# Kernel optimization log

Hardware: AMD Instinct MI355X
Metric: run time of the kernel (lower is better)

## Reference

```python
import jax, jax.numpy as jnp
import numpy as np

NEG_INF = -1.0e9  # matches torch masked_fill value (unused: no mask)

def setup_inputs() -> dict:
    key = jax.random.key(0)
    kq, kk, kv = jax.random.split(key, 3)
    B, Sq, Sk, D = 8, 2048, 2048, 512
    return {
        "query": jax.random.normal(kq, (B, Sq, D), dtype=jnp.float32),
        "key": jax.random.normal(kk, (B, Sk, D), dtype=jnp.float32),
        "value": jax.random.normal(kv, (B, Sk, D), dtype=jnp.float32),
        "temperature": jnp.ones((), dtype=jnp.float32),
    }

def reference(query, key, value, temperature):
    # Squared Euclidean distance via GEMM identity: ||q||^2 + ||k||^2 - 2 q.k
    # (same math as the broadcast sum((q-k)^2, -1), but without [B,Sq,Sk,D] tensor)
    q_sq = jnp.sum(query * query, axis=-1, keepdims=True)          # [B,Sq,1]
    k_sq = jnp.sum(key * key, axis=-1)[:, None, :]                 # [B,1,Sk]
    qk = jnp.einsum("bqd,bkd->bqk", query, key)                    # [B,Sq,Sk]
    distance_squared = q_sq + k_sq - 2.0 * qk
    similarity = -distance_squared / temperature
    attention_weights = jax.nn.softmax(similarity, axis=-1)        # [B,Sq,Sk]
    attended_values = jnp.einsum("bqk,bkd->bqd", attention_weights, value)
    return attended_values, attention_weights
```

## Files before the change

kernel.cpp:

```cpp
#include <hip/hip_runtime.h>

typedef __bf16 bf16_t;
typedef __bf16 bf16x8 __attribute__((ext_vector_type(8)));
typedef __bf16 bf16x4 __attribute__((ext_vector_type(4)));
typedef __bf16 bf16x2 __attribute__((ext_vector_type(2)));
typedef float f32x4 __attribute__((ext_vector_type(4)));

#define NB 8
#define SQ 2048
#define SK 2048
#define DD 512

#define BM 128
#define BN 128
#define BK 32
#define LDK 40
#define NBLK (SK / BN)

__global__ __launch_bounds__(256, 2) void logits_kernel(
    const float* __restrict__ Q, const float* __restrict__ K,
    const float* __restrict__ tempP, float* __restrict__ logits,
    float* __restrict__ Mpart, float* __restrict__ Spart) {
  __shared__ bf16_t qh[BM][LDK], ql[BM][LDK], kh[BN][LDK], kl[BN][LDK];
  __shared__ float ksred[BN][8];
  __shared__ float mred[BM][2], sred[BM][2];
  const int b = blockIdx.z;
  const int m0 = blockIdx.y * BM;
  const int n0 = blockIdx.x * BN;
  const int tid = threadIdx.x;
  const int lane = tid & 63;
  const int wave = tid >> 6;
  const int wm = (wave >> 1) * 64;
  const int wn = (wave & 1) * 64;
  const int lrow = lane & 15;
  const int quad = lane >> 4;

  const float* Qb = Q + (size_t)b * SQ * DD;
  const float* Kb = K + (size_t)b * SK * DD;

  const int srow = tid >> 3;
  const int scol = (tid & 7) * 4;

  const float* qbase = Qb + (size_t)(m0 + srow) * DD + scol;
  const float* kbase = Kb + (size_t)(n0 + srow) * DD + scol;

  f32x4 acc[4][4];
#pragma unroll
  for (int i = 0; i < 4; i++)
#pragma unroll
    for (int j = 0; j < 4; j++) acc[i][j] = (f32x4){0.f, 0.f, 0.f, 0.f};

  float kss[4] = {0.f, 0.f, 0.f, 0.f};

  float4 pq[4], pk[4];
#pragma unroll
  for (int i = 0; i < 4; i++) {
    pq[i] = *(const float4*)(qbase + (size_t)i * 32 * DD);
    pk[i] = *(const float4*)(kbase + (size_t)i * 32 * DD);
  }

  for (int k0 = 0; k0 < DD; k0 += BK) {
    __syncthreads();
#pragma unroll
    for (int i = 0; i < 4; i++) {
      const int r = srow + i * 32;
      float4 qv = pq[i], kv = pk[i];
      bf16_t q0 = (bf16_t)qv.x, q1 = (bf16_t)qv.y, q2 = (bf16_t)qv.z, q3 = (bf16_t)qv.w;
      bf16x4 qhv = {q0, q1, q2, q3};
      bf16x4 qlv = {(bf16_t)(qv.x - (float)q0), (bf16_t)(qv.y - (float)q1),
                    (bf16_t)(qv.z - (float)q2), (bf16_t)(qv.w - (float)q3)};
      bf16_t c0 = (bf16_t)kv.x, c1 = (bf16_t)kv.y, c2 = (bf16_t)kv.z, c3 = (bf16_t)kv.w;
      bf16x4 khv = {c0, c1, c2, c3};
      bf16x4 klv = {(bf16_t)(kv.x - (float)c0), (bf16_t)(kv.y - (float)c1),
                    (bf16_t)(kv.z - (float)c2), (bf16_t)(kv.w - (float)c3)};
      *(bf16x4*)&qh[r][scol] = qhv;
      *(bf16x4*)&ql[r][scol] = qlv;
      *(bf16x4*)&kh[r][scol] = khv;
      *(bf16x4*)&kl[r][scol] = klv;
      kss[i] = fmaf(kv.x, kv.x, kss[i]);
      kss[i] = fmaf(kv.y, kv.y, kss[i]);
      kss[i] = fmaf(kv.z, kv.z, kss[i]);
      kss[i] = fmaf(kv.w, kv.w, kss[i]);
    }
    __syncthreads();

    if (k0 + BK < DD) {
#pragma unroll
      for (int i = 0; i < 4; i++) {
        pq[i] = *(const float4*)(qbase + (size_t)i * 32 * DD + (k0 + BK));
        pk[i] = *(const float4*)(kbase + (size_t)i * 32 * DD + (k0 + BK));
      }
    }

    bf16x8 bh[4], bl[4];
#pragma unroll
    for (int ni = 0; ni < 4; ni++) {
      bh[ni] = *(const bf16x8*)&kh[wn + ni * 16 + lrow][quad * 8];
      bl[ni] = *(const bf16x8*)&kl[wn + ni * 16 + lrow][quad * 8];
    }
#pragma unroll
    for (int mi = 0; mi < 4; mi++) {
      bf16x8 ah = *(const bf16x8*)&qh[wm + mi * 16 + lrow][quad * 8];
      bf16x8 al = *(const bf16x8*)&ql[wm + mi * 16 + lrow][quad * 8];
#pragma unroll
      for (int ni = 0; ni < 4; ni++) {
        acc[mi][ni] = __builtin_amdgcn_mfma_f32_16x16x32_bf16(ah, bh[ni], acc[mi][ni], 0, 0, 0);
        acc[mi][ni] = __builtin_amdgcn_mfma_f32_16x16x32_bf16(ah, bl[ni], acc[mi][ni], 0, 0, 0);
        acc[mi][ni] = __builtin_amdgcn_mfma_f32_16x16x32_bf16(al, bh[ni], acc[mi][ni], 0, 0, 0);
      }
    }
  }

#pragma unroll
  for (int i = 0; i < 4; i++) ksred[srow + i * 32][tid & 7] = kss[i];
  __syncthreads();

  const float invT = 1.0f / tempP[0];
  float* Lb = logits + (size_t)b * SQ * SK;
  float ks4[4];
#pragma unroll
  for (int ni = 0; ni < 4; ni++) {
    const float* kr = ksred[wn + ni * 16 + lrow];
    ks4[ni] = ((kr[0] + kr[1]) + (kr[2] + kr[3])) +
              ((kr[4] + kr[5]) + (kr[6] + kr[7]));
  }

#pragma unroll
  for (int mi = 0; mi < 4; mi++) {
#pragma unroll
    for (int r = 0; r < 4; r++) {
      const int row = wm + mi * 16 + quad * 4 + r;
      float sv[4];
#pragma unroll
      for (int ni = 0; ni < 4; ni++) {
        sv[ni] = (2.0f * acc[mi][ni][r] - ks4[ni]) * invT;
        Lb[(size_t)(m0 + row) * SK + (n0 + wn + ni * 16 + lrow)] = sv[ni];
      }
      float rm = fmaxf(fmaxf(sv[0], sv[1]), fmaxf(sv[2], sv[3]));
      rm = fmaxf(rm, __shfl_xor(rm, 1));
      rm = fmaxf(rm, __shfl_xor(rm, 2));
      rm = fmaxf(rm, __shfl_xor(rm, 4));
      rm = fmaxf(rm, __shfl_xor(rm, 8));
      float rs = __expf(sv[0] - rm) + __expf(sv[1] - rm) +
                 __expf(sv[2] - rm) + __expf(sv[3] - rm);
      rs += __shfl_xor(rs, 1);
      rs += __shfl_xor(rs, 2);
      rs += __shfl_xor(rs, 4);
      rs += __shfl_xor(rs, 8);
      if (lrow == 0) {
        mred[row][wave & 1] = rm;
        sred[row][wave & 1] = rs;
      }
    }
  }
  __syncthreads();
  if (tid < BM) {
    const float ma = mred[tid][0], mb = mred[tid][1];
    const float M = fmaxf(ma, mb);
    const float S = sred[tid][0] * __expf(ma - M) + sred[tid][1] * __expf(mb - M);
    const size_t o = ((size_t)b * NBLK + blockIdx.x) * SQ + (m0 + tid);
    Mpart[o] = M;
    Spart[o] = S;
  }
}

__global__ __launch_bounds__(256) void vt_kernel(const float* __restrict__ V,
                                                 bf16_t* __restrict__ Vt) {
  const int b = blockIdx.y;
  const int k0 = blockIdx.x * 32;
  const int tid = threadIdx.x;
  const int p = tid & 15;
  const int c = tid >> 4;
  const float* Vb = V + (size_t)b * SK * DD;
  bf16_t* Vtb = Vt + (size_t)b * DD * SK;
  const int k = k0 + 2 * p;
#pragma unroll
  for (int j = 0; j < 8; j++) {
    const int d0 = 4 * c + 64 * j;
    float4 v0 = *(const float4*)(Vb + (size_t)k * DD + d0);
    float4 v1 = *(const float4*)(Vb + (size_t)(k + 1) * DD + d0);
    bf16x2 t0 = {(bf16_t)v0.x, (bf16_t)v1.x};
    bf16x2 t1 = {(bf16_t)v0.y, (bf16_t)v1.y};
    bf16x2 t2 = {(bf16_t)v0.z, (bf16_t)v1.z};
    bf16x2 t3 = {(bf16_t)v0.w, (bf16_t)v1.w};
    *(bf16x2*)(Vtb + (size_t)(d0 + 0) * SK + k) = t0;
    *(bf16x2*)(Vtb + (size_t)(d0 + 1) * SK + k) = t1;
    *(bf16x2*)(Vtb + (size_t)(d0 + 2) * SK + k) = t2;
    *(bf16x2*)(Vtb + (size_t)(d0 + 3) * SK + k) = t3;
  }
}

#define PM 32

__device__ __forceinline__ unsigned lds_addr(int row, unsigned kb) {
  return (unsigned)row * 4096u + (kb ^ (unsigned)((row & 7) << 4));
}

__global__ __launch_bounds__(512, 1) void pv_kernel(
    float* __restrict__ L,
    const bf16_t* __restrict__ Vt,
    const float* __restrict__ Mpart, const float* __restrict__ Spart,
    float* __restrict__ O) {
  __shared__ __align__(16) unsigned char wlds[PM * 4096];
  __shared__ float Msh[PM], Ssh[PM];
  const int bid = blockIdx.x;
  const int b = bid & 7;
  const int m0 = (bid >> 3) * PM;
  const int tid = threadIdx.x;

  float* Lb = L + (size_t)b * SQ * SK;
  const bf16_t* Vtb = Vt + (size_t)b * DD * SK;

  {
    const int row = tid >> 4;
    const int j = tid & 15;
    const size_t o = ((size_t)b * NBLK + j) * SQ + (m0 + row);
    const float pm = Mpart[o];
    const float ps = Spart[o];
    float m = pm;
    m = fmaxf(m, __shfl_xor(m, 1));
    m = fmaxf(m, __shfl_xor(m, 2));
    m = fmaxf(m, __shfl_xor(m, 4));
    m = fmaxf(m, __shfl_xor(m, 8));
    float s = ps * __expf(pm - m);
    s += __shfl_xor(s, 1);
    s += __shfl_xor(s, 2);
    s += __shfl_xor(s, 4);
    s += __shfl_xor(s, 8);
    if (j == 0) {
      Msh[row] = m;
      Ssh[row] = 1.0f / s;
    }
  }
  __syncthreads();

  {
    const int row = tid >> 4;
    const int g = tid & 15;
    float* lp = Lb + (size_t)(m0 + row) * SK;
    const float M = Msh[row];
    const float invS = Ssh[row];
#pragma unroll 8
    for (int j = 0; j < 32; j++) {
      const int k = g * 4 + j * 64;
      float4 v = *(const float4*)(lp + k);
      const float w0 = __expf(v.x - M) * invS;
      const float w1 = __expf(v.y - M) * invS;
      const float w2 = __expf(v.z - M) * invS;
      const float w3 = __expf(v.w - M) * invS;
      *(float4*)(lp + k) = make_float4(w0, w1, w2, w3);
      bf16x4 w4 = {(bf16_t)w0, (bf16_t)w1, (bf16_t)w2, (bf16_t)w3};
      *(bf16x4*)(wlds + lds_addr(row, (unsigned)(k * 2))) = w4;
    }
  }
  __syncthreads();

  const int lane = tid & 63;
  const int wave = tid >> 6;
  const int wn = wave * 64;
  const int lrow = lane & 15;
  const int quad = lane >> 4;

  const bf16_t* Brow[4];
#pragma unroll
  for (int ni = 0; ni < 4; ni++)
    Brow[ni] = Vtb + (size_t)(wn + ni * 16 + lrow) * SK + quad * 8;

  f32x4 acc[2][4];
#pragma unroll
  for (int i = 0; i < 2; i++)
#pragma unroll
    for (int j = 0; j < 4; j++) acc[i][j] = (f32x4){0.f, 0.f, 0.f, 0.f};

  bf16x8 b0[4], b1[4];
#pragma unroll
  for (int ni = 0; ni < 4; ni++) b0[ni] = *(const bf16x8*)(Brow[ni]);
#pragma unroll
  for (int ni = 0; ni < 4; ni++) b1[ni] = *(const bf16x8*)(Brow[ni] + BK);

  for (int k0 = 0; k0 < SK; k0 += 2 * BK) {
    bf16x8 a0[2], a1[2];
#pragma unroll
    for (int mi = 0; mi < 2; mi++) {
      const int row = mi * 16 + lrow;
      a0[mi] = *(const bf16x8*)(wlds + lds_addr(row, (unsigned)((k0 + quad * 8) * 2)));
      a1[mi] = *(const bf16x8*)(wlds + lds_addr(row, (unsigned)((k0 + BK + quad * 8) * 2)));
    }
#pragma unroll
    for (int mi = 0; mi < 2; mi++)
#pragma unroll
      for (int ni = 0; ni < 4; ni++)
        acc[mi][ni] = __builtin_amdgcn_mfma_f32_16x16x32_bf16(a0[mi], b0[ni],
                                                              acc[mi][ni], 0, 0, 0);
    if (k0 + 2 * BK < SK) {
#pragma unroll
      for (int ni = 0; ni < 4; ni++)
        b0[ni] = *(const bf16x8*)(Brow[ni] + k0 + 2 * BK);
    }
#pragma unroll
    for (int mi = 0; mi < 2; mi++)
#pragma unroll
      for (int ni = 0; ni < 4; ni++)
        acc[mi][ni] = __builtin_amdgcn_mfma_f32_16x16x32_bf16(a1[mi], b1[ni],
                                                              acc[mi][ni], 0, 0, 0);
    if (k0 + 3 * BK < SK) {
#pragma unroll
      for (int ni = 0; ni < 4; ni++)
        b1[ni] = *(const bf16x8*)(Brow[ni] + k0 + 3 * BK);
    }
  }

  float* Ob = O + (size_t)b * SQ * DD;
#pragma unroll
  for (int ni = 0; ni < 4; ni++) {
    const int d = wn + ni * 16 + lrow;
#pragma unroll
    for (int mi = 0; mi < 2; mi++) {
      const int mbase = m0 + mi * 16 + quad * 4;
#pragma unroll
      for (int r = 0; r < 4; r++) {
        Ob[(size_t)(mbase + r) * DD + d] = acc[mi][ni][r];
      }
    }
  }
}

extern "C" void kernel_launch(void* const* d_in, const int* in_sizes, int n_in,
                              void* d_out, int out_size, void* d_ws, size_t ws_size,
                              hipStream_t stream) {
  const float* Q = (const float*)d_in[0];
  const float* K = (const float*)d_in[1];
  const float* V = (const float*)d_in[2];
  const float* T = (const float*)d_in[3];

  float* outv = (float*)d_out;
  float* logits = outv + (size_t)NB * SQ * DD;

  float* Mpart = (float*)d_ws;
  float* Spart = Mpart + (size_t)NB * NBLK * SQ;
  bf16_t* Vt = (bf16_t*)(Spart + (size_t)NB * NBLK * SQ);

  vt_kernel<<<dim3(SK / 32, NB), 256, 0, stream>>>(V, Vt);
  logits_kernel<<<dim3(SK / BN, SQ / BM, NB), 256, 0, stream>>>(Q, K, T, logits,
                                                                Mpart, Spart);
  pv_kernel<<<dim3(NB * (SQ / PM)), 512, 0, stream>>>(logits, Vt, Mpart, Spart, outv);
}
```

Baseline: 474.5 us.

## Pipeline softmax normalization with PV MFMA using chunked double-buffered LDS

The PV kernel no longer normalizes a whole 2048-wide row into a 128KB LDS buffer before any MFMA work. It now processes 256-wide chunks with a double-buffered 32KB LDS tile, prefetching the next chunk's logits while computing MFMAs on the current one, so global reads overlap with compute. The smaller LDS footprint allows more blocks per CU (launch bounds raised to 4). Logits are also pre-scaled by log2(e) so exp2f can replace __expf, at the cost of a log2-scaled intermediate and a hand-written barrier.

```diff
diff --git a/kernel.cpp b/kernel.cpp
--- a/kernel.cpp
+++ b/kernel.cpp
@@ -115,7 +115,7 @@
   for (int i = 0; i < 4; i++) ksred[srow + i * 32][tid & 7] = kss[i];
   __syncthreads();
 
-  const float invT = 1.0f / tempP[0];
+  const float invT = 1.4426950408889634f / tempP[0];
   float* Lb = logits + (size_t)b * SQ * SK;
   float ks4[4];
 #pragma unroll
@@ -141,8 +141,8 @@
       rm = fmaxf(rm, __shfl_xor(rm, 2));
       rm = fmaxf(rm, __shfl_xor(rm, 4));
       rm = fmaxf(rm, __shfl_xor(rm, 8));
-      float rs = __expf(sv[0] - rm) + __expf(sv[1] - rm) +
-                 __expf(sv[2] - rm) + __expf(sv[3] - rm);
+      float rs = exp2f(sv[0] - rm) + exp2f(sv[1] - rm) +
+                 exp2f(sv[2] - rm) + exp2f(sv[3] - rm);
       rs += __shfl_xor(rs, 1);
       rs += __shfl_xor(rs, 2);
       rs += __shfl_xor(rs, 4);
@@ -157,7 +157,7 @@
   if (tid < BM) {
     const float ma = mred[tid][0], mb = mred[tid][1];
     const float M = fmaxf(ma, mb);
-    const float S = sred[tid][0] * __expf(ma - M) + sred[tid][1] * __expf(mb - M);
+    const float S = sred[tid][0] * exp2f(ma - M) + sred[tid][1] * exp2f(mb - M);
     const size_t o = ((size_t)b * NBLK + blockIdx.x) * SQ + (m0 + tid);
     Mpart[o] = M;
     Spart[o] = S;
@@ -191,17 +191,21 @@
 }
 
 #define PM 32
-
-__device__ __forceinline__ unsigned lds_addr(int row, unsigned kb) {
-  return (unsigned)row * 4096u + (kb ^ (unsigned)((row & 7) << 4));
-}
-
-__global__ __launch_bounds__(512, 1) void pv_kernel(
+#define CK 256
+#define CKB 512
+#define NCH (SK / CK)
+#define NWIN (SK / BK)
+
+__device__ __forceinline__ unsigned pv_lds(int row, unsigned kb) {
+  return (unsigned)row * CKB + (kb ^ (unsigned)((row & 7) << 4));
+}
+
+__global__ __launch_bounds__(512, 4) void pv_kernel(
     float* __restrict__ L,
     const bf16_t* __restrict__ Vt,
     const float* __restrict__ Mpart, const float* __restrict__ Spart,
     float* __restrict__ O) {
-  __shared__ __align__(16) unsigned char wlds[PM * 4096];
+  __shared__ __align__(16) unsigned char wlds[2][PM * CKB];
   __shared__ float Msh[PM], Ssh[PM];
   const int bid = blockIdx.x;
   const int b = bid & 7;
@@ -222,7 +226,7 @@
     m = fmaxf(m, __shfl_xor(m, 2));
     m = fmaxf(m, __shfl_xor(m, 4));
     m = fmaxf(m, __shfl_xor(m, 8));
-    float s = ps * __expf(pm - m);
+    float s = ps * exp2f(pm - m);
     s += __shfl_xor(s, 1);
     s += __shfl_xor(s, 2);
     s += __shfl_xor(s, 4);
@@ -234,26 +238,28 @@
   }
   __syncthreads();
 
-  {
-    const int row = tid >> 4;
-    const int g = tid & 15;
-    float* lp = Lb + (size_t)(m0 + row) * SK;
-    const float M = Msh[row];
-    const float invS = Ssh[row];
-#pragma unroll 8
-    for (int j = 0; j < 32; j++) {
+  const int prow = tid >> 4;
+  const int g = tid & 15;
+  float* lp = Lb + (size_t)(m0 + prow) * SK;
+  const float Mrow = Msh[prow];
+  const float invS = Ssh[prow];
+
+  auto stage = [&](const float4 (&pv4)[4], int c1) {
+    unsigned char* buf = wlds[c1 & 1];
+    const int kbase = c1 * CK;
+#pragma unroll
+    for (int j = 0; j < 4; j++) {
       const int k = g * 4 + j * 64;
-      float4 v = *(const float4*)(lp + k);
-      const float w0 = __expf(v.x - M) * invS;
-      const float w1 = __expf(v.y - M) * invS;
-      const float w2 = __expf(v.z - M) * invS;
-      const float w3 = __expf(v.w - M) * invS;
-      *(float4*)(lp + k) = make_float4(w0, w1, w2, w3);
+      float4 v = pv4[j];
+      const float w0 = exp2f(v.x - Mrow) * invS;
+      const float w1 = exp2f(v.y - Mrow) * invS;
+      const float w2 = exp2f(v.z - Mrow) * invS;
+      const float w3 = exp2f(v.w - Mrow) * invS;
+      *(float4*)(lp + kbase + k) = make_float4(w0, w1, w2, w3);
       bf16x4 w4 = {(bf16_t)w0, (bf16_t)w1, (bf16_t)w2, (bf16_t)w3};
-      *(bf16x4*)(wlds + lds_addr(row, (unsigned)(k * 2))) = w4;
-    }
-  }
-  __syncthreads();
+      *(bf16x4*)(buf + pv_lds(prow, (unsigned)(k * 2))) = w4;
+    }
+  };
 
   const int lane = tid & 63;
   const int wave = tid >> 6;
@@ -272,41 +278,52 @@
 #pragma unroll
     for (int j = 0; j < 4; j++) acc[i][j] = (f32x4){0.f, 0.f, 0.f, 0.f};
 
-  bf16x8 b0[4], b1[4];
-#pragma unroll
-  for (int ni = 0; ni < 4; ni++) b0[ni] = *(const bf16x8*)(Brow[ni]);
-#pragma unroll
-  for (int ni = 0; ni < 4; ni++) b1[ni] = *(const bf16x8*)(Brow[ni] + BK);
-
-  for (int k0 = 0; k0 < SK; k0 += 2 * BK) {
-    bf16x8 a0[2], a1[2];
-#pragma unroll
-    for (int mi = 0; mi < 2; mi++) {
-      const int row = mi * 16 + lrow;
-      a0[mi] = *(const bf16x8*)(wlds + lds_addr(row, (unsigned)((k0 + quad * 8) * 2)));
-      a1[mi] = *(const bf16x8*)(wlds + lds_addr(row, (unsigned)((k0 + BK + quad * 8) * 2)));
-    }
-#pragma unroll
-    for (int mi = 0; mi < 2; mi++)
+  {
+    float4 p0[4];
+#pragma unroll
+    for (int j = 0; j < 4; j++) p0[j] = *(const float4*)(lp + g * 4 + j * 64);
+    stage(p0, 0);
+  }
+  bf16x8 bw[2][4];
+#pragma unroll
+  for (int ni = 0; ni < 4; ni++) bw[0][ni] = *(const bf16x8*)(Brow[ni]);
+#pragma unroll
+  for (int ni = 0; ni < 4; ni++) bw[1][ni] = *(const bf16x8*)(Brow[ni] + BK);
+  __syncthreads();
+
+  for (int c = 0; c < NCH; c++) {
+    float4 pn[4];
+    if (c + 1 < NCH) {
+      const int kbase = (c + 1) * CK;
+#pragma unroll
+      for (int j = 0; j < 4; j++)
+        pn[j] = *(const float4*)(lp + kbase + g * 4 + j * 64);
+    }
+
+    const unsigned char* buf = wlds[c & 1];
+#pragma unroll
+    for (int w = 0; w < CK / BK; w++) {
+      const int gw = c * (CK / BK) + w;
+      bf16x8 a0 = *(const bf16x8*)(buf + pv_lds(lrow, (unsigned)(w * 64 + quad * 16)));
+      bf16x8 a1 = *(const bf16x8*)(buf + pv_lds(16 + lrow, (unsigned)(w * 64 + quad * 16)));
 #pragma unroll
       for (int ni = 0; ni < 4; ni++)
-        acc[mi][ni] = __builtin_amdgcn_mfma_f32_16x16x32_bf16(a0[mi], b0[ni],
-                                                              acc[mi][ni], 0, 0, 0);
-    if (k0 + 2 * BK < SK) {
+        acc[0][ni] = __builtin_amdgcn_mfma_f32_16x16x32_bf16(a0, bw[gw & 1][ni],
+                                                             acc[0][ni], 0, 0, 0);
 #pragma unroll
       for (int ni = 0; ni < 4; ni++)
-        b0[ni] = *(const bf16x8*)(Brow[ni] + k0 + 2 * BK);
-    }
-#pragma unroll
-    for (int mi = 0; mi < 2; mi++)
-#pragma unroll
-      for (int ni = 0; ni < 4; ni++)
-        acc[mi][ni] = __builtin_amdgcn_mfma_f32_16x16x32_bf16(a1[mi], b1[ni],
-                                                              acc[mi][ni], 0, 0, 0);
-    if (k0 + 3 * BK < SK) {
-#pragma unroll
-      for (int ni = 0; ni < 4; ni++)
-        b1[ni] = *(const bf16x8*)(Brow[ni] + k0 + 3 * BK);
+        acc[1][ni] = __builtin_amdgcn_mfma_f32_16x16x32_bf16(a1, bw[gw & 1][ni],
+                                                             acc[1][ni], 0, 0, 0);
+      if (gw + 2 < NWIN) {
+#pragma unroll
+        for (int ni = 0; ni < 4; ni++)
+          bw[gw & 1][ni] = *(const bf16x8*)(Brow[ni] + (gw + 2) * BK);
+      }
+    }
+
+    if (c + 1 < NCH) {
+      stage(pn, c + 1);
+      asm volatile("s_waitcnt lgkmcnt(0)\n\ts_barrier" ::: "memory");
     }
   }
 
```

Measured after the change: 460.0 us. 3.1% less time.
